# Kernel tuning notes

Measured on AMD Instinct MI355X. Metric: run time of the kernel, lower is better.

The kernel has to match this reference:

```python
import jax, jax.numpy as jnp
import numpy as np

T, H, I, SI, E, K = 1024, 2048, 1408, 5632, 8, 4
NORM_TOPK_PROB = False


def setup_inputs() -> dict:
    key = jax.random.key(0)
    ks = jax.random.split(key, 9)
    s = lambda k, shape, fan: (jax.random.normal(k, shape, jnp.float32) * (fan ** -0.5))
    return {
        "hidden_states": jax.random.normal(ks[0], (T, H), jnp.float32),
        "Wg": s(ks[1], (E, H, I), H),   # per-expert gate_proj
        "Wu": s(ks[2], (E, H, I), H),   # per-expert up_proj
        "Wd": s(ks[3], (E, I, H), I),   # per-expert down_proj
        "Wsg": s(ks[4], (H, SI), H),    # shared expert gate_proj
        "Wsu": s(ks[5], (H, SI), H),    # shared expert up_proj
        "Wsd": s(ks[6], (SI, H), SI),   # shared expert down_proj
        "W_router": s(ks[7], (H, E), H),        # self.gate
        "W_shared_gate": s(ks[8], (H, 1), H),   # self.shared_expert_gate
    }


def reference(hidden_states, Wg, Wu, Wd, Wsg, Wsu, Wsd, W_router, W_shared_gate):
    x = hidden_states  # [T, H]
    # shared expert: silu(x Wg) * (x Wu) then down proj (fused_gate_up + matmul)
    shared = (jax.nn.silu(x @ Wsg) * (x @ Wsu)) @ Wsd          # [T, H]
    shared_gate = jax.nn.sigmoid(x @ W_shared_gate)            # [T, 1]
    # router: softmax in float32, then top-k
    probs = jax.nn.softmax((x @ W_router).astype(jnp.float32), axis=-1)  # [T, E]
    top_v, top_i = jax.lax.top_k(probs, K)                     # [T, K]
    if NORM_TOPK_PROB and K > 1:
        top_v = top_v / jnp.sum(top_v, axis=-1, keepdims=True)
    # combine weights: zero for non-routed (expert, token) pairs -> same math
    # as the original gather/expert/scatter(index_add_) loop
    combine = jnp.zeros((T, E), top_v.dtype).at[jnp.arange(T)[:, None], top_i].set(top_v)
    # expert GEMMs (dequantized-GPTQ math): silu(x Wg_e) * (x Wu_e) @ Wd_e
    g = jnp.einsum('th,ehi->eti', x, Wg)                       # [E, T, I]
    u = jnp.einsum('th,ehi->eti', x, Wu)                       # [E, T, I]
    y = jnp.einsum('eti,eih->eth', jax.nn.silu(g) * u, Wd)     # [E, T, H]
    moe = jnp.einsum('eth,te->th', y, combine.astype(x.dtype)) # [T, H]
    scale = 1.0 / (K ** 0.5)
    return (moe + shared_gate * shared) * jnp.asarray(scale, x.dtype)
```

## Files before the change

kernel.cpp:

```cpp
#include <hip/hip_runtime.h>
#include <cstdint>
#include <cstddef>


typedef unsigned short u16;
typedef _Float16 f16;
typedef __attribute__((ext_vector_type(8))) _Float16 half8;
typedef __attribute__((ext_vector_type(4))) float f32x4;

__device__ __forceinline__ float b2f(u16 u){ return __uint_as_float(((uint32_t)u)<<16); }
__device__ __forceinline__ u16 f2b(float f){
  uint32_t x = __float_as_uint(f);
  return (u16)((x + 0x7fffu + ((x>>16)&1u)) >> 16);
}
template<bool F32> __device__ __forceinline__ float ldf(const void* p, size_t i){
  if (F32) return ((const float*)p)[i];
  else     return b2f(((const u16*)p)[i]);
}

__global__ __launch_bounds__(64) void detect_kernel(const uint32_t* __restrict__ X,
                                                    int* __restrict__ flag){
  const int lane = threadIdx.x;
  int cnt = 0;
  for (int i = lane; i < 256; i += 64){
    const uint32_t e = (X[i] >> 23) & 0xffu;
    cnt += (e >= 90u && e <= 160u) ? 1 : 0;
  }
#pragma unroll
  for (int off = 32; off > 0; off >>= 1) cnt += __shfl_xor(cnt, off, 64);
  if (lane == 0) *flag = (cnt > 128) ? 1 : 0;
}

template<bool F32>
__device__ void router_body(const void* X, const void* Wr, const void* Wxg,
                            float* __restrict__ combine, float* __restrict__ sgate){
  const int t = blockIdx.x;
  const int lane = threadIdx.x;
  float acc[8] = {0,0,0,0,0,0,0,0};
  float ag = 0.f;
#pragma unroll
  for (int j = 0; j < 4; ++j){
    const int h0 = j*512 + lane*8;
#pragma unroll
    for (int jj = 0; jj < 8; ++jj){
      const int h = h0 + jj;
      const float xv = ldf<F32>(X, (size_t)t*2048 + h);
#pragma unroll
      for (int e = 0; e < 8; ++e) acc[e] += xv * ldf<F32>(Wr, (size_t)h*8 + e);
      ag += xv * ldf<F32>(Wxg, (size_t)h);
    }
  }
#pragma unroll
  for (int off = 32; off > 0; off >>= 1){
#pragma unroll
    for (int e = 0; e < 8; ++e) acc[e] += __shfl_xor(acc[e], off, 64);
    ag += __shfl_xor(ag, off, 64);
  }
  if (lane == 0){
    float m = acc[0];
#pragma unroll
    for (int e = 1; e < 8; ++e) m = fmaxf(m, acc[e]);
    float p[8]; float s = 0.f;
#pragma unroll
    for (int e = 0; e < 8; ++e){ p[e] = __expf(acc[e]-m); s += p[e]; }
    const float inv = 1.f/s;
#pragma unroll
    for (int e = 0; e < 8; ++e) p[e] *= inv;
#pragma unroll
    for (int e = 0; e < 8; ++e){
      int cnt = 0;
#pragma unroll
      for (int j = 0; j < 8; ++j)
        cnt += (p[j] > p[e]) || (p[j] == p[e] && j < e);
      combine[(size_t)t*8 + e] = (cnt < 4) ? p[e] : 0.f;
    }
    sgate[t] = 1.f/(1.f + __expf(-ag));
  }
}
__global__ __launch_bounds__(64) void router_kernel(const void* X, const void* Wr, const void* Wxg,
                                                    float* combine, float* sgate, const int* flag){
  if (*flag) router_body<true >(X, Wr, Wxg, combine, sgate);
  else       router_body<false>(X, Wr, Wxg, combine, sgate);
}

__global__ __launch_bounds__(256) void xconvert(const void* __restrict__ X,
                                                f16* __restrict__ Xh, const int* flag){
  const int i = (blockIdx.x*256 + threadIdx.x)*8;
  half8 h;
  if (*flag){
    const float* p = (const float*)X + i;
    const float4 a = *(const float4*)p;
    const float4 b = *(const float4*)(p+4);
    h[0]=(f16)a.x; h[1]=(f16)a.y; h[2]=(f16)a.z; h[3]=(f16)a.w;
    h[4]=(f16)b.x; h[5]=(f16)b.y; h[6]=(f16)b.z; h[7]=(f16)b.w;
  } else {
    union { uint4 v; u16 s[8]; } r;
    r.v = *(const uint4*)((const u16*)X + i);
#pragma unroll
    for (int q = 0; q < 8; ++q) h[q] = (f16)b2f(r.s[q]);
  }
  *(half8*)(Xh + i) = h;
}

#define TP 72
template<bool F32>
__device__ void tcvt_body(const void* S, f16* __restrict__ D, int K, int N,
                          size_t sstride, size_t dstride, f16* Tt){
  const int z = blockIdx.z;
  const int n0 = blockIdx.x*64, k0 = blockIdx.y*64;
  const int t = threadIdx.x;
  f16* Dm = D + (size_t)z*dstride;
  const int kr = t >> 4, nc = (t & 15)*4;
#pragma unroll
  for (int p = 0; p < 4; ++p){
    const int kk = p*16 + kr;
    float v0, v1, v2, v3;
    if (F32){
      const float* Sm = (const float*)S + (size_t)z*sstride;
      const float4 v = *(const float4*)(Sm + (size_t)(k0+kk)*N + n0 + nc);
      v0=v.x; v1=v.y; v2=v.z; v3=v.w;
    } else {
      const u16* Sm = (const u16*)S + (size_t)z*sstride;
      union { uint2 u; u16 s[4]; } r;
      r.u = *(const uint2*)(Sm + (size_t)(k0+kk)*N + n0 + nc);
      v0=b2f(r.s[0]); v1=b2f(r.s[1]); v2=b2f(r.s[2]); v3=b2f(r.s[3]);
    }
    Tt[(nc+0)*TP + kk] = (f16)v0;
    Tt[(nc+1)*TP + kk] = (f16)v1;
    Tt[(nc+2)*TP + kk] = (f16)v2;
    Tt[(nc+3)*TP + kk] = (f16)v3;
  }
  __syncthreads();
  const int nr = t >> 3, kc = (t & 7)*8;
#pragma unroll
  for (int p = 0; p < 2; ++p){
    const int n = p*32 + nr;
    const half8 v = *(const half8*)(Tt + n*TP + kc);
    *(half8*)(Dm + (size_t)(n0+n)*K + k0 + kc) = v;
  }
}
__global__ __launch_bounds__(256) void tcvt(const void* S, f16* D, int K, int N,
                                            size_t sstride, size_t dstride, const int* flag){
  __shared__ f16 Tt[64*TP];
  if (*flag) tcvt_body<true >(S, D, K, N, sstride, dstride, Tt);
  else       tcvt_body<false>(S, D, K, N, sstride, dstride, Tt);
}

__device__ __forceinline__ void stage_T128(const f16* __restrict__ Row, int ld, int k0, f16* Ls){
  const int tid = threadIdx.x, wave = tid>>6, lane = tid&63;
#pragma unroll
  for (int i = 0; i < 2; ++i){
    const int rbase = i*64 + wave*16;
    const f16* g = Row + (size_t)(rbase + (lane>>2))*ld + (k0 + (lane&3)*8);
    __builtin_amdgcn_global_load_lds((const __attribute__((address_space(1))) void*)g,
                                     (__attribute__((address_space(3))) void*)(Ls + rbase*32),
                                     16, 0, 0);
  }
}
__device__ __forceinline__ void stage_T64(const f16* __restrict__ Row, int ld, int k0, f16* Ls){
  const int tid = threadIdx.x, wave = tid>>6, lane = tid&63;
  const int rbase = wave*16;
  const f16* g = Row + (size_t)(rbase + (lane>>2))*ld + (k0 + (lane&3)*8);
  __builtin_amdgcn_global_load_lds((const __attribute__((address_space(1))) void*)g,
                                   (__attribute__((address_space(3))) void*)(Ls + rbase*32),
                                   16, 0, 0);
}

__global__ __launch_bounds__(256) void gu_gemm_t(
    const f16* __restrict__ Xh, const f16* __restrict__ WsgT, const f16* __restrict__ WsuT,
    const f16* __restrict__ WgT, const f16* __restrict__ WuT,
    f16* __restrict__ A1s, f16* __restrict__ P,
    const float* __restrict__ sgate, const float* __restrict__ combine)
{
  __shared__ f16 As[128*32];
  __shared__ f16 Bg[64*32];
  __shared__ f16 Bu[64*32];
  int bid = blockIdx.x;
  const f16 *BgRow, *BuRow; f16* outp; const float* rs;
  int rs_stride, ldout, m0, n0;
  if (bid < 704){
    n0 = (bid % 88)*64; m0 = (bid / 88)*128;
    BgRow = WsgT + (size_t)n0*2048; BuRow = WsuT + (size_t)n0*2048;
    outp = A1s; rs = sgate; rs_stride = 1; ldout = 5632;
  } else {
    bid -= 704;
    const int e = bid / 176, r = bid % 176;
    n0 = (r % 22)*64; m0 = (r / 22)*128;
    const size_t off = (size_t)e*1408*2048;
    BgRow = WgT + off + (size_t)n0*2048; BuRow = WuT + off + (size_t)n0*2048;
    outp = P + (size_t)e*1408; rs = combine + e; rs_stride = 8; ldout = 11264;
  }
  const f16* Arow = Xh + (size_t)m0*2048;
  const int tid = threadIdx.x, lane = tid&63, wave = tid>>6;
  const int wm = wave>>1, wn = wave&1, lr = lane&15, q = lane>>4;

  const f32x4 z4 = {0.f,0.f,0.f,0.f};
  f32x4 ag[4][2], au[4][2];
#pragma unroll
  for (int mi = 0; mi < 4; ++mi)
#pragma unroll
    for (int ni = 0; ni < 2; ++ni){ ag[mi][ni] = z4; au[mi][ni] = z4; }

  for (int k0 = 0; k0 < 2048; k0 += 32){
    __syncthreads();
    stage_T128(Arow, 2048, k0, As);
    stage_T64(BgRow, 2048, k0, Bg);
    stage_T64(BuRow, 2048, k0, Bu);
    __syncthreads();
    half8 af[4];
#pragma unroll
    for (int mi = 0; mi < 4; ++mi)
      af[mi] = *(const half8*)(As + (wm*64 + mi*16 + lr)*32 + q*8);
#pragma unroll
    for (int ni = 0; ni < 2; ++ni){
      const half8 bfg = *(const half8*)(Bg + (wn*32 + ni*16 + lr)*32 + q*8);
      const half8 bfu = *(const half8*)(Bu + (wn*32 + ni*16 + lr)*32 + q*8);
#pragma unroll
      for (int mi = 0; mi < 4; ++mi){
        ag[mi][ni] = __builtin_amdgcn_mfma_f32_16x16x32_f16(af[mi], bfg, ag[mi][ni], 0, 0, 0);
        au[mi][ni] = __builtin_amdgcn_mfma_f32_16x16x32_f16(af[mi], bfu, au[mi][ni], 0, 0, 0);
      }
    }
  }

  float rsv[4][4];
#pragma unroll
  for (int mi = 0; mi < 4; ++mi)
#pragma unroll
    for (int r = 0; r < 4; ++r)
      rsv[mi][r] = rs[(size_t)(m0 + wm*64 + mi*16 + q*4 + r)*rs_stride];
#pragma unroll
  for (int mi = 0; mi < 4; ++mi)
#pragma unroll
    for (int ni = 0; ni < 2; ++ni)
#pragma unroll
      for (int r = 0; r < 4; ++r){
        const int row = m0 + wm*64 + mi*16 + q*4 + r;
        const int col = n0 + wn*32 + ni*16 + lr;
        const float g = ag[mi][ni][r];
        const float v = (g / (1.f + __expf(-g))) * au[mi][ni][r] * rsv[mi][r];
        outp[(size_t)row*ldout + col] = (f16)v;
      }
}

__global__ __launch_bounds__(256) void down_gemm_t(
    const f16* __restrict__ Pm, const f16* __restrict__ A1s,
    const f16* __restrict__ WdT, const f16* __restrict__ WsdT,
    float* __restrict__ part)
{
  __shared__ f16 As[128*32];
  __shared__ f16 Bs[128*32];
  const int z = blockIdx.z;
  const f16 *A, *B; int lda, ldk;
  if (z < 4){ A = Pm + (size_t)z*2816;     lda = 11264; B = WdT  + (size_t)z*2816;     ldk = 11264; }
  else      { A = A1s + (size_t)(z-4)*2816; lda = 5632; B = WsdT + (size_t)(z-4)*2816; ldk = 5632; }
  float* C = part + (size_t)z*2097152;
  const int m0 = blockIdx.y*128, n0 = blockIdx.x*128;
  const f16* Arow = A + (size_t)m0*lda;
  const f16* Brow = B + (size_t)n0*ldk;
  const int tid = threadIdx.x, lane = tid&63, wave = tid>>6;
  const int wm = wave>>1, wn = wave&1, lr = lane&15, q = lane>>4;

  const f32x4 z4 = {0.f,0.f,0.f,0.f};
  f32x4 acc[4][4];
#pragma unroll
  for (int mi = 0; mi < 4; ++mi)
#pragma unroll
    for (int ni = 0; ni < 4; ++ni) acc[mi][ni] = z4;

  for (int kt = 0; kt < 88; ++kt){
    __syncthreads();
    stage_T128(Arow, lda, kt*32, As);
    stage_T128(Brow, ldk, kt*32, Bs);
    __syncthreads();
    half8 af[4], bf[4];
#pragma unroll
    for (int mi = 0; mi < 4; ++mi)
      af[mi] = *(const half8*)(As + (wm*64 + mi*16 + lr)*32 + q*8);
#pragma unroll
    for (int ni = 0; ni < 4; ++ni)
      bf[ni] = *(const half8*)(Bs + (wn*64 + ni*16 + lr)*32 + q*8);
#pragma unroll
    for (int ni = 0; ni < 4; ++ni)
#pragma unroll
      for (int mi = 0; mi < 4; ++mi)
        acc[mi][ni] = __builtin_amdgcn_mfma_f32_16x16x32_f16(af[mi], bf[ni], acc[mi][ni], 0, 0, 0);
  }
#pragma unroll
  for (int mi = 0; mi < 4; ++mi)
#pragma unroll
    for (int ni = 0; ni < 4; ++ni)
#pragma unroll
      for (int r = 0; r < 4; ++r){
        const int row = m0 + wm*64 + mi*16 + q*4 + r;
        const int col = n0 + wn*64 + ni*16 + lr;
        C[(size_t)row*2048 + col] = acc[mi][ni][r];
      }
}

__global__ __launch_bounds__(256) void final6(const float4* __restrict__ part,
                                              void* __restrict__ out, const int* flag, int n4){
  const int i = blockIdx.x*256 + threadIdx.x;
  if (i >= n4) return;
  float v0 = 0.f, v1 = 0.f, v2 = 0.f, v3 = 0.f;
#pragma unroll
  for (int z = 0; z < 6; ++z){
    const float4 a = part[(size_t)z*524288 + i];
    v0 += a.x; v1 += a.y; v2 += a.z; v3 += a.w;
  }
  v0 *= 0.5f; v1 *= 0.5f; v2 *= 0.5f; v3 *= 0.5f;
  if (*flag){
    float4 o; o.x=v0; o.y=v1; o.z=v2; o.w=v3;
    ((float4*)out)[i] = o;
  } else {
    uint2 o;
    o.x = (uint32_t)f2b(v0) | ((uint32_t)f2b(v1) << 16);
    o.y = (uint32_t)f2b(v2) | ((uint32_t)f2b(v3) << 16);
    ((uint2*)out)[i] = o;
  }
}

#define LDBT 40
#define ABUF 4096
#define BBUF 2560
struct BR { float v[8]; };
template<bool F32>
__device__ __forceinline__ void loadB(const void* __restrict__ B, size_t ldb, int k0, int n0, BR& r){
  const int t = threadIdx.x, c = t&63, kg = t>>6;
  if (F32){
    const float* p = (const float*)B + (size_t)(k0 + kg*8)*ldb + (n0 + c);
#pragma unroll
    for (int j = 0; j < 8; ++j) r.v[j] = p[(size_t)j*ldb];
  } else {
    const u16* p = (const u16*)B + (size_t)(k0 + kg*8)*ldb + (n0 + c);
#pragma unroll
    for (int j = 0; j < 8; ++j) r.v[j] = b2f(p[(size_t)j*ldb]);
  }
}
__device__ __forceinline__ void storeB(const BR& r, f16* BT){
  const int t = threadIdx.x, c = t&63, kg = t>>6;
  half8 h;
#pragma unroll
  for (int j = 0; j < 8; ++j) h[j] = (f16)r.v[j];
  *(half8*)(BT + c*LDBT + kg*8) = h;
}
template<bool F32>
__device__ void gu_body_r(const f16* __restrict__ Arow, const void* __restrict__ Bgp,
                          const void* __restrict__ Bup, f16* __restrict__ outp,
                          const float* __restrict__ rs, int rs_stride,
                          int ldb, int ldout, int m0, int n0,
                          f16* As, f16* BgT, f16* BuT)
{
  const int tid = threadIdx.x, lane = tid&63, wave = tid>>6;
  const int wm = wave>>1, wn = wave&1, lr = lane&15, q = lane>>4;
  const f32x4 z4 = {0.f,0.f,0.f,0.f};
  f32x4 ag[4][2], au[4][2];
#pragma unroll
  for (int mi = 0; mi < 4; ++mi)
#pragma unroll
    for (int ni = 0; ni < 2; ++ni){ ag[mi][ni] = z4; au[mi][ni] = z4; }
  const int KT = 64;
  BR rg, ru;
  loadB<F32>(Bgp, ldb, 0, n0, rg);
  loadB<F32>(Bup, ldb, 0, n0, ru);
  storeB(rg, BgT); storeB(ru, BuT);
  stage_T128(Arow, 2048, 0, As);
  loadB<F32>(Bgp, ldb, 32, n0, rg);
  loadB<F32>(Bup, ldb, 32, n0, ru);
  __syncthreads();
  for (int kt = 0; kt < KT; ++kt){
    const int cur = kt&1, nxt = cur^1;
    if (kt+1 < KT){
      storeB(rg, BgT + nxt*BBUF);
      storeB(ru, BuT + nxt*BBUF);
      stage_T128(Arow, 2048, (kt+1)*32, As + nxt*ABUF);
    }
    if (kt+2 < KT){
      loadB<F32>(Bgp, ldb, (kt+2)*32, n0, rg);
      loadB<F32>(Bup, ldb, (kt+2)*32, n0, ru);
    }
    const f16* Ac = As + cur*ABUF;
    const f16* Bgc = BgT + cur*BBUF;
    const f16* Buc = BuT + cur*BBUF;
    half8 af[4];
#pragma unroll
    for (int mi = 0; mi < 4; ++mi)
      af[mi] = *(const half8*)(Ac + (wm*64 + mi*16 + lr)*32 + q*8);
#pragma unroll
    for (int ni = 0; ni < 2; ++ni){
      const half8 bfg = *(const half8*)(Bgc + (wn*32 + ni*16 + lr)*LDBT + q*8);
      const half8 bfu = *(const half8*)(Buc + (wn*32 + ni*16 + lr)*LDBT + q*8);
#pragma unroll
      for (int mi = 0; mi < 4; ++mi){
        ag[mi][ni] = __builtin_amdgcn_mfma_f32_16x16x32_f16(af[mi], bfg, ag[mi][ni], 0, 0, 0);
        au[mi][ni] = __builtin_amdgcn_mfma_f32_16x16x32_f16(af[mi], bfu, au[mi][ni], 0, 0, 0);
      }
    }
    __syncthreads();
  }
  float rsv[4][4];
#pragma unroll
  for (int mi = 0; mi < 4; ++mi)
#pragma unroll
    for (int r = 0; r < 4; ++r)
      rsv[mi][r] = rs[(size_t)(m0 + wm*64 + mi*16 + q*4 + r)*rs_stride];
#pragma unroll
  for (int mi = 0; mi < 4; ++mi)
#pragma unroll
    for (int ni = 0; ni < 2; ++ni)
#pragma unroll
      for (int r = 0; r < 4; ++r){
        const int row = m0 + wm*64 + mi*16 + q*4 + r;
        const int col = n0 + wn*32 + ni*16 + lr;
        const float g = ag[mi][ni][r];
        const float v = (g / (1.f + __expf(-g))) * au[mi][ni][r] * rsv[mi][r];
        outp[(size_t)row*ldout + col] = (f16)v;
      }
}
__global__ __launch_bounds__(256) void gu_gemm_r(
    const f16* __restrict__ Xh, const void* Wsg, const void* Wsu,
    const void* Wg, const void* Wu, f16* __restrict__ A1s, f16* __restrict__ P,
    const float* __restrict__ sgate, const float* __restrict__ combine, const int* flag)
{
  __shared__ f16 As[2*ABUF];
  __shared__ f16 BgT[2*BBUF];
  __shared__ f16 BuT[2*BBUF];
  const bool f32v = (*flag != 0);
  int bid = blockIdx.x;
  const void *Bg, *Bu; f16* outp; const float* rs;
  int rs_stride, ldb, ldout, m0, n0;
  if (bid < 704){
    n0 = (bid % 88)*64; m0 = (bid / 88)*128;
    Bg = Wsg; Bu = Wsu; outp = A1s; rs = sgate;
    rs_stride = 1; ldb = 5632; ldout = 5632;
  } else {
    bid -= 704;
    const int e = bid / 176, r = bid % 176;
    n0 = (r % 22)*64; m0 = (r / 22)*128;
    const size_t off = (size_t)e*2048*1408;
    Bg = f32v ? (const void*)((const float*)Wg + off) : (const void*)((const u16*)Wg + off);
    Bu = f32v ? (const void*)((const float*)Wu + off) : (const void*)((const u16*)Wu + off);
    outp = P + (size_t)e*1408; rs = combine + e;
    rs_stride = 8; ldb = 1408; ldout = 11264;
  }
  const f16* Arow = Xh + (size_t)m0*2048;
  if (f32v) gu_body_r<true >(Arow, Bg, Bu, outp, rs, rs_stride, ldb, ldout, m0, n0, As, BgT, BuT);
  else      gu_body_r<false>(Arow, Bg, Bu, outp, rs, rs_stride, ldb, ldout, m0, n0, As, BgT, BuT);
}
template<bool F32>
__device__ void down_body_r(const f16* __restrict__ Arow, int lda, const void* __restrict__ B,
                            float* __restrict__ C, int m0, int n0, f16* As, f16* BT)
{
  const int tid = threadIdx.x, lane = tid&63, wave = tid>>6;
  const int wm = wave>>1, wn = wave&1, lr = lane&15, q = lane>>4;
  const f32x4 z4 = {0.f,0.f,0.f,0.f};
  f32x4 acc[4][2];
#pragma unroll
  for (int mi = 0; mi < 4; ++mi)
#pragma unroll
    for (int ni = 0; ni < 2; ++ni) acc[mi][ni] = z4;
  const int KT = 176;
  BR rb;
  loadB<F32>(B, 2048, 0, n0, rb);
  storeB(rb, BT);
  stage_T128(Arow, lda, 0, As);
  loadB<F32>(B, 2048, 32, n0, rb);
  __syncthreads();
  for (int kt = 0; kt < KT; ++kt){
    const int cur = kt&1, nxt = cur^1;
    if (kt+1 < KT){
      storeB(rb, BT + nxt*BBUF);
      stage_T128(Arow, lda, (kt+1)*32, As + nxt*ABUF);
    }
    if (kt+2 < KT) loadB<F32>(B, 2048, (kt+2)*32, n0, rb);
    const f16* Ac = As + cur*ABUF;
    const f16* Bc = BT + cur*BBUF;
    half8 af[4];
#pragma unroll
    for (int mi = 0; mi < 4; ++mi)
      af[mi] = *(const half8*)(Ac + (wm*64 + mi*16 + lr)*32 + q*8);
#pragma unroll
    for (int ni = 0; ni < 2; ++ni){
      const half8 bf = *(const half8*)(Bc + (wn*32 + ni*16 + lr)*LDBT + q*8);
#pragma unroll
      for (int mi = 0; mi < 4; ++mi)
        acc[mi][ni] = __builtin_amdgcn_mfma_f32_16x16x32_f16(af[mi], bf, acc[mi][ni], 0, 0, 0);
    }
    __syncthreads();
  }
#pragma unroll
  for (int mi = 0; mi < 4; ++mi)
#pragma unroll
    for (int ni = 0; ni < 2; ++ni)
#pragma unroll
      for (int r = 0; r < 4; ++r){
        const int row = m0 + wm*64 + mi*16 + q*4 + r;
        const int col = n0 + wn*32 + ni*16 + lr;
        C[(size_t)row*2048 + col] = acc[mi][ni][r];
      }
}
__global__ __launch_bounds__(256) void down_gemm_r(
    const f16* __restrict__ Pm, const f16* __restrict__ A1s,
    const void* Wd, const void* Wsd,
    float* __restrict__ c0, float* __restrict__ c1, float* __restrict__ c2, const int* flag)
{
  __shared__ f16 As[2*ABUF];
  __shared__ f16 BT[2*BBUF];
  const int z = blockIdx.z;
  const bool f32v = (*flag != 0);
  const f16* A; const void* B; float* C; int lda;
  if (z == 0){ A = Pm; B = Wd; C = c0; lda = 11264; }
  else if (z == 1){
    A = Pm + 5632;
    B = f32v ? (const void*)((const float*)Wd + (size_t)5632*2048)
             : (const void*)((const u16*)Wd + (size_t)5632*2048);
    C = c1; lda = 11264;
  } else { A = A1s; B = Wsd; C = c2; lda = 5632; }
  const int m0 = blockIdx.y*128, n0 = blockIdx.x*64;
  const f16* Arow = A + (size_t)m0*lda;
  if (f32v) down_body_r<true >(Arow, lda, B, C, m0, n0, As, BT);
  else      down_body_r<false>(Arow, lda, B, C, m0, n0, As, BT);
}
__global__ __launch_bounds__(256) void final3(
    const float4* __restrict__ b0, const float4* __restrict__ b1, const float4* __restrict__ b2,
    void* __restrict__ out, const int* flag, int n4){
  const int i = blockIdx.x*256 + threadIdx.x;
  if (i >= n4) return;
  const float4 a = b0[i], b = b1[i], c = b2[i];
  const float v0 = 0.5f*(a.x + b.x + c.x);
  const float v1 = 0.5f*(a.y + b.y + c.y);
  const float v2 = 0.5f*(a.z + b.z + c.z);
  const float v3 = 0.5f*(a.w + b.w + c.w);
  if (*flag){
    float4 o; o.x=v0; o.y=v1; o.z=v2; o.w=v3;
    ((float4*)out)[i] = o;
  } else {
    uint2 o;
    o.x = (uint32_t)f2b(v0) | ((uint32_t)f2b(v1) << 16);
    o.y = (uint32_t)f2b(v2) | ((uint32_t)f2b(v3) << 16);
    ((uint2*)out)[i] = o;
  }
}

extern "C" void kernel_launch(void* const* d_in, const int* in_sizes, int n_in,
                              void* d_out, int out_size, void* d_ws, size_t ws_size,
                              hipStream_t stream)
{
  (void)in_sizes; (void)n_in; (void)out_size;
  const void* x   = d_in[0];
  const void* Wg  = d_in[1];
  const void* Wu  = d_in[2];
  const void* Wd  = d_in[3];
  const void* Wsg = d_in[4];
  const void* Wsu = d_in[5];
  const void* Wsd = d_in[6];
  const void* Wr  = d_in[7];
  const void* Wxg = d_in[8];

  char* ws = (char*)d_ws;
  size_t off = 0;
  auto alloc = [&](size_t bytes)->char*{
    char* p = ws + off; off = (off + bytes + 255) & ~(size_t)255; return p;
  };
  float* combine = (float*)alloc(32768);
  float* sgate   = (float*)alloc(4096);
  int*   flag    = (int*)  alloc(4096);
  f16*   Xh      = (f16*)  alloc((size_t)1024*2048*2);
  f16*   A1s     = (f16*)  alloc((size_t)1024*5632*2);
  f16*   P       = (f16*)  alloc((size_t)1024*11264*2);
  float* part    = (float*)alloc((size_t)6*2097152*4);
  f16*   WsgT    = (f16*)  alloc((size_t)5632*2048*2);
  f16*   WsuT    = (f16*)  alloc((size_t)5632*2048*2);
  f16*   WgT     = (f16*)  alloc((size_t)8*1408*2048*2);
  f16*   WuT     = (f16*)  alloc((size_t)8*1408*2048*2);
  f16*   WdT     = (f16*)  alloc((size_t)2048*11264*2);
  f16*   WsdT    = (f16*)  alloc((size_t)2048*5632*2);
  const size_t NEED_FULL = off;

  detect_kernel<<<dim3(1), dim3(64), 0, stream>>>((const uint32_t*)x, flag);
  router_kernel<<<dim3(1024), dim3(64), 0, stream>>>(x, Wr, Wxg, combine, sgate, flag);
  xconvert<<<dim3(1024), dim3(256), 0, stream>>>(x, Xh, flag);

  if (ws_size >= NEED_FULL){
    tcvt<<<dim3(88, 32, 1), dim3(256), 0, stream>>>(Wsg, WsgT, 2048, 5632, 0, 0, flag);
    tcvt<<<dim3(88, 32, 1), dim3(256), 0, stream>>>(Wsu, WsuT, 2048, 5632, 0, 0, flag);
    tcvt<<<dim3(22, 32, 8), dim3(256), 0, stream>>>(Wg, WgT, 2048, 1408,
        (size_t)2048*1408, (size_t)2048*1408, flag);
    tcvt<<<dim3(22, 32, 8), dim3(256), 0, stream>>>(Wu, WuT, 2048, 1408,
        (size_t)2048*1408, (size_t)2048*1408, flag);
    tcvt<<<dim3(32, 176, 1), dim3(256), 0, stream>>>(Wd, WdT, 11264, 2048, 0, 0, flag);
    tcvt<<<dim3(32, 88, 1), dim3(256), 0, stream>>>(Wsd, WsdT, 5632, 2048, 0, 0, flag);

    gu_gemm_t<<<dim3(2112), dim3(256), 0, stream>>>(
        Xh, WsgT, WsuT, WgT, WuT, A1s, P, sgate, combine);
    down_gemm_t<<<dim3(16, 8, 6), dim3(256), 0, stream>>>(P, A1s, WdT, WsdT, part);
    final6<<<dim3(2048), dim3(256), 0, stream>>>((const float4*)part, d_out, flag, 524288);
  } else {
    float* b0 = part;
    float* b1 = part + 2097152;
    float* b2 = part + 2*2097152;
    gu_gemm_r<<<dim3(2112), dim3(256), 0, stream>>>(
        Xh, Wsg, Wsu, Wg, Wu, A1s, P, sgate, combine, flag);
    down_gemm_r<<<dim3(32, 8, 3), dim3(256), 0, stream>>>(P, A1s, Wd, Wsd, b0, b1, b2, flag);
    final3<<<dim3(2048), dim3(256), 0, stream>>>(
        (const float4*)b0, (const float4*)b1, (const float4*)b2, d_out, flag, 524288);
  }
}
```

Measured before the change: 826.0 us.

## Compact routed tokens per expert and skip GEMM tiles for unrouted tokens

```diff
diff --git a/kernel.cpp b/kernel.cpp
--- a/kernel.cpp
+++ b/kernel.cpp
@@ -81,6 +81,34 @@
                                                     float* combine, float* sgate, const int* flag){
   if (*flag) router_body<true >(X, Wr, Wxg, combine, sgate);
   else       router_body<false>(X, Wr, Wxg, combine, sgate);
+}
+
+__global__ __launch_bounds__(1024) void compact_kernel(
+    const float* __restrict__ combine, int* __restrict__ cnt,
+    int* __restrict__ tok, float* __restrict__ cw, int* __restrict__ inv){
+  __shared__ int lc[8];
+  const int t = threadIdx.x;
+  if (t < 8) lc[t] = 0;
+  __syncthreads();
+  int k = 0;
+#pragma unroll
+  for (int e = 0; e < 8; ++e){
+    const float v = combine[(size_t)t*8 + e];
+    if (v > 0.f){
+      const int p = atomicAdd(&lc[e], 1);
+      tok[e*1024 + p] = t;
+      cw [e*1024 + p] = v;
+      if (k < 4) inv[t*4 + k] = e*1024 + p;
+      ++k;
+    }
+  }
+  for (; k < 4; ++k) inv[t*4 + k] = -1;
+  __syncthreads();
+#pragma unroll
+  for (int e = 0; e < 8; ++e){
+    if (t >= lc[e]){ tok[e*1024 + t] = 0; cw[e*1024 + t] = 0.f; }
+  }
+  if (t < 8) cnt[t] = lc[t];
 }
 
 __global__ __launch_bounds__(256) void xconvert(const void* __restrict__ X,
@@ -170,28 +198,39 @@
     const f16* __restrict__ Xh, const f16* __restrict__ WsgT, const f16* __restrict__ WsuT,
     const f16* __restrict__ WgT, const f16* __restrict__ WuT,
     f16* __restrict__ A1s, f16* __restrict__ P,
-    const float* __restrict__ sgate, const float* __restrict__ combine)
+    const float* __restrict__ sgate, const float* __restrict__ cw,
+    const int* __restrict__ cnt, const int* __restrict__ tok)
 {
   __shared__ f16 As[128*32];
   __shared__ f16 Bg[64*32];
   __shared__ f16 Bu[64*32];
   int bid = blockIdx.x;
+  const int tid = threadIdx.x, lane = tid&63, wave = tid>>6;
   const f16 *BgRow, *BuRow; f16* outp; const float* rs;
-  int rs_stride, ldout, m0, n0;
+  int ldout, m0, n0;
+  const f16 *gA0, *gA1;
   if (bid < 704){
     n0 = (bid % 88)*64; m0 = (bid / 88)*128;
     BgRow = WsgT + (size_t)n0*2048; BuRow = WsuT + (size_t)n0*2048;
-    outp = A1s; rs = sgate; rs_stride = 1; ldout = 5632;
+    outp = A1s; rs = sgate; ldout = 5632;
+    const int r0 = m0 + wave*16 + (lane>>2);
+    gA0 = Xh + (size_t)r0*2048 + (lane&3)*8;
+    gA1 = gA0 + (size_t)64*2048;
   } else {
     bid -= 704;
     const int e = bid / 176, r = bid % 176;
-    n0 = (r % 22)*64; m0 = (r / 22)*128;
+    const int mt = r / 22;
+    if (mt*128 >= cnt[e]) return;
+    n0 = (r % 22)*64; m0 = mt*128;
     const size_t off = (size_t)e*1408*2048;
     BgRow = WgT + off + (size_t)n0*2048; BuRow = WuT + off + (size_t)n0*2048;
-    outp = P + (size_t)e*1408; rs = combine + e; rs_stride = 8; ldout = 11264;
-  }
-  const f16* Arow = Xh + (size_t)m0*2048;
-  const int tid = threadIdx.x, lane = tid&63, wave = tid>>6;
+    outp = P + (size_t)e*1024*1408; rs = cw + e*1024; ldout = 1408;
+    const int* tp = tok + e*1024 + m0;
+    const int t0 = tp[wave*16 + (lane>>2)];
+    const int t1 = tp[64 + wave*16 + (lane>>2)];
+    gA0 = Xh + (size_t)t0*2048 + (lane&3)*8;
+    gA1 = Xh + (size_t)t1*2048 + (lane&3)*8;
+  }
   const int wm = wave>>1, wn = wave&1, lr = lane&15, q = lane>>4;
 
   const f32x4 z4 = {0.f,0.f,0.f,0.f};
@@ -203,7 +242,12 @@
 
   for (int k0 = 0; k0 < 2048; k0 += 32){
     __syncthreads();
-    stage_T128(Arow, 2048, k0, As);
+    __builtin_amdgcn_global_load_lds((const __attribute__((address_space(1))) void*)(gA0 + k0),
+                                     (__attribute__((address_space(3))) void*)(As + (wave*16)*32),
+                                     16, 0, 0);
+    __builtin_amdgcn_global_load_lds((const __attribute__((address_space(1))) void*)(gA1 + k0),
+                                     (__attribute__((address_space(3))) void*)(As + (64 + wave*16)*32),
+                                     16, 0, 0);
     stage_T64(BgRow, 2048, k0, Bg);
     stage_T64(BuRow, 2048, k0, Bu);
     __syncthreads();
@@ -228,7 +272,7 @@
   for (int mi = 0; mi < 4; ++mi)
 #pragma unroll
     for (int r = 0; r < 4; ++r)
-      rsv[mi][r] = rs[(size_t)(m0 + wm*64 + mi*16 + q*4 + r)*rs_stride];
+      rsv[mi][r] = rs[m0 + wm*64 + mi*16 + q*4 + r];
 #pragma unroll
   for (int mi = 0; mi < 4; ++mi)
 #pragma unroll
@@ -246,17 +290,25 @@
 __global__ __launch_bounds__(256) void down_gemm_t(
     const f16* __restrict__ Pm, const f16* __restrict__ A1s,
     const f16* __restrict__ WdT, const f16* __restrict__ WsdT,
-    float* __restrict__ part)
+    const int* __restrict__ cnt,
+    float* __restrict__ downR, float* __restrict__ shp)
 {
   __shared__ f16 As[128*32];
   __shared__ f16 Bs[128*32];
   const int z = blockIdx.z;
-  const f16 *A, *B; int lda, ldk;
-  if (z < 4){ A = Pm + (size_t)z*2816;     lda = 11264; B = WdT  + (size_t)z*2816;     ldk = 11264; }
-  else      { A = A1s + (size_t)(z-4)*2816; lda = 5632; B = WsdT + (size_t)(z-4)*2816; ldk = 5632; }
-  float* C = part + (size_t)z*2097152;
   const int m0 = blockIdx.y*128, n0 = blockIdx.x*128;
-  const f16* Arow = A + (size_t)m0*lda;
+  const f16 *A, *B; int lda, ldk, KT; float* C;
+  if (z < 8){
+    if (m0 >= cnt[z]) return;
+    A = Pm + (size_t)z*1024*1408 + (size_t)m0*1408; lda = 1408;
+    B = WdT + (size_t)z*1408; ldk = 11264; KT = 44;
+    C = downR + (size_t)z*1024*2048;
+  } else {
+    A = A1s + (size_t)(z-8)*2816 + (size_t)m0*5632; lda = 5632;
+    B = WsdT + (size_t)(z-8)*2816; ldk = 5632; KT = 88;
+    C = shp + (size_t)(z-8)*2097152;
+  }
+  const f16* Arow = A;
   const f16* Brow = B + (size_t)n0*ldk;
   const int tid = threadIdx.x, lane = tid&63, wave = tid>>6;
   const int wm = wave>>1, wn = wave&1, lr = lane&15, q = lane>>4;
@@ -268,7 +320,7 @@
 #pragma unroll
     for (int ni = 0; ni < 4; ++ni) acc[mi][ni] = z4;
 
-  for (int kt = 0; kt < 88; ++kt){
+  for (int kt = 0; kt < KT; ++kt){
     __syncthreads();
     stage_T128(Arow, lda, kt*32, As);
     stage_T128(Brow, ldk, kt*32, Bs);
@@ -298,25 +350,36 @@
       }
 }
 
-__global__ __launch_bounds__(256) void final6(const float4* __restrict__ part,
-                                              void* __restrict__ out, const int* flag, int n4){
-  const int i = blockIdx.x*256 + threadIdx.x;
-  if (i >= n4) return;
-  float v0 = 0.f, v1 = 0.f, v2 = 0.f, v3 = 0.f;
-#pragma unroll
-  for (int z = 0; z < 6; ++z){
-    const float4 a = part[(size_t)z*524288 + i];
-    v0 += a.x; v1 += a.y; v2 += a.z; v3 += a.w;
-  }
-  v0 *= 0.5f; v1 *= 0.5f; v2 *= 0.5f; v3 *= 0.5f;
-  if (*flag){
-    float4 o; o.x=v0; o.y=v1; o.z=v2; o.w=v3;
-    ((float4*)out)[i] = o;
-  } else {
-    uint2 o;
-    o.x = (uint32_t)f2b(v0) | ((uint32_t)f2b(v1) << 16);
-    o.y = (uint32_t)f2b(v2) | ((uint32_t)f2b(v3) << 16);
-    ((uint2*)out)[i] = o;
+__global__ __launch_bounds__(256) void final_g(
+    const float4* __restrict__ sh0, const float4* __restrict__ sh1,
+    const float4* __restrict__ downR, const int* __restrict__ inv,
+    void* __restrict__ out, const int* __restrict__ flag){
+  const int t = blockIdx.x;
+  const int4 iv = *(const int4*)(inv + t*4);
+  const int idx[4] = {iv.x, iv.y, iv.z, iv.w};
+#pragma unroll
+  for (int jj = 0; jj < 2; ++jj){
+    const int j = threadIdx.x + jj*256;
+    const size_t b = (size_t)t*512 + j;
+    const float4 a = sh0[b], c = sh1[b];
+    float v0 = a.x + c.x, v1 = a.y + c.y, v2 = a.z + c.z, v3 = a.w + c.w;
+#pragma unroll
+    for (int k = 0; k < 4; ++k){
+      if (idx[k] >= 0){
+        const float4 d = downR[(size_t)idx[k]*512 + j];
+        v0 += d.x; v1 += d.y; v2 += d.z; v3 += d.w;
+      }
+    }
+    v0 *= 0.5f; v1 *= 0.5f; v2 *= 0.5f; v3 *= 0.5f;
+    if (*flag){
+      float4 o; o.x=v0; o.y=v1; o.z=v2; o.w=v3;
+      ((float4*)out)[b] = o;
+    } else {
+      uint2 o;
+      o.x = (uint32_t)f2b(v0) | ((uint32_t)f2b(v1) << 16);
+      o.y = (uint32_t)f2b(v2) | ((uint32_t)f2b(v3) << 16);
+      ((uint2*)out)[b] = o;
+    }
   }
 }
 
@@ -565,10 +628,15 @@
   float* combine = (float*)alloc(32768);
   float* sgate   = (float*)alloc(4096);
   int*   flag    = (int*)  alloc(4096);
+  int*   cnt     = (int*)  alloc(4096);
+  int*   tok     = (int*)  alloc(8*1024*4);
+  float* cw      = (float*)alloc(8*1024*4);
+  int*   inv     = (int*)  alloc(1024*4*4);
   f16*   Xh      = (f16*)  alloc((size_t)1024*2048*2);
   f16*   A1s     = (f16*)  alloc((size_t)1024*5632*2);
-  f16*   P       = (f16*)  alloc((size_t)1024*11264*2);
-  float* part    = (float*)alloc((size_t)6*2097152*4);
+  f16*   P       = (f16*)  alloc((size_t)8*1024*1408*2);
+  float* shp     = (float*)alloc((size_t)3*2097152*4);
+  float* downR   = (float*)alloc((size_t)8*1024*2048*4);
   f16*   WsgT    = (f16*)  alloc((size_t)5632*2048*2);
   f16*   WsuT    = (f16*)  alloc((size_t)5632*2048*2);
   f16*   WgT     = (f16*)  alloc((size_t)8*1408*2048*2);
@@ -582,6 +650,7 @@
   xconvert<<<dim3(1024), dim3(256), 0, stream>>>(x, Xh, flag);
 
   if (ws_size >= NEED_FULL){
+    compact_kernel<<<dim3(1), dim3(1024), 0, stream>>>(combine, cnt, tok, cw, inv);
     tcvt<<<dim3(88, 32, 1), dim3(256), 0, stream>>>(Wsg, WsgT, 2048, 5632, 0, 0, flag);
     tcvt<<<dim3(88, 32, 1), dim3(256), 0, stream>>>(Wsu, WsuT, 2048, 5632, 0, 0, flag);
     tcvt<<<dim3(22, 32, 8), dim3(256), 0, stream>>>(Wg, WgT, 2048, 1408,
@@ -592,13 +661,15 @@
     tcvt<<<dim3(32, 88, 1), dim3(256), 0, stream>>>(Wsd, WsdT, 5632, 2048, 0, 0, flag);
 
     gu_gemm_t<<<dim3(2112), dim3(256), 0, stream>>>(
-        Xh, WsgT, WsuT, WgT, WuT, A1s, P, sgate, combine);
-    down_gemm_t<<<dim3(16, 8, 6), dim3(256), 0, stream>>>(P, A1s, WdT, WsdT, part);
-    final6<<<dim3(2048), dim3(256), 0, stream>>>((const float4*)part, d_out, flag, 524288);
+        Xh, WsgT, WsuT, WgT, WuT, A1s, P, sgate, cw, cnt, tok);
+    down_gemm_t<<<dim3(16, 8, 10), dim3(256), 0, stream>>>(P, A1s, WdT, WsdT, cnt, downR, shp);
+    final_g<<<dim3(1024), dim3(256), 0, stream>>>(
+        (const float4*)shp, (const float4*)(shp + 2097152), (const float4*)downR,
+        inv, d_out, flag);
   } else {
-    float* b0 = part;
-    float* b1 = part + 2097152;
-    float* b2 = part + 2*2097152;
+    float* b0 = shp;
+    float* b1 = shp + 2097152;
+    float* b2 = shp + 2*2097152;
     gu_gemm_r<<<dim3(2112), dim3(256), 0, stream>>>(
         Xh, Wsg, Wsu, Wg, Wu, A1s, P, sgate, combine, flag);
     down_gemm_r<<<dim3(32, 8, 3), dim3(256), 0, stream>>>(P, A1s, Wd, Wsd, b0, b1, b2, flag);
```

New measurement: 700.2 us. 1.18x faster.
